# Kernel optimization log

Measured on AMD Instinct MI355X. Metric: run time of the kernel, lower is better.

Reference implementation:

```python
import jax, jax.numpy as jnp
import numpy as np

WS = 7      # window size
SHIFT = 3   # shift size
H = 56
W = 56
NH = 16     # num heads


def _layernorm(x, g, b):
    m = x.mean(-1, keepdims=True)
    v = x.var(-1, keepdims=True)
    return (x - m) / jnp.sqrt(v + 1e-5) * g + b


def setup_inputs() -> dict:
    key = jax.random.key(0)
    ks = jax.random.split(key, 8)
    B, C = 16, 512
    DH = 4 * C
    s = 0.02
    x = jax.random.normal(ks[0], (B, H * W, C), jnp.float32)

    # relative position index (matches torch buffer construction)
    coords = np.stack(np.meshgrid(np.arange(WS), np.arange(WS), indexing='ij')).reshape(2, -1)
    rel = (coords[:, :, None] - coords[:, None, :]).transpose(1, 2, 0).copy()
    rel[..., 0] += WS - 1
    rel[..., 1] += WS - 1
    rel[..., 0] *= 2 * WS - 1
    rpi = jnp.asarray(rel.sum(-1), jnp.int32)  # (49, 49)

    # shifted-window additive attention mask (nW, N, N)
    img = np.zeros((H, W))
    cnt = 0
    for hs in (slice(0, -WS), slice(-WS, -SHIFT), slice(-SHIFT, None)):
        for wsl in (slice(0, -WS), slice(-WS, -SHIFT), slice(-SHIFT, None)):
            img[hs, wsl] = cnt
            cnt += 1
    mw = img.reshape(H // WS, WS, W // WS, WS).transpose(0, 2, 1, 3).reshape(-1, WS * WS)
    diff = mw[:, None, :] - mw[:, :, None]  # == mw.unsqueeze(1) - mw.unsqueeze(2)
    attn_mask = jnp.asarray(np.where(diff != 0, -100.0, 0.0), jnp.float32)

    return {
        'x': x,
        'rpi': rpi,
        'attn_mask': attn_mask,
        'norm1_g': jnp.ones((C,), jnp.float32),
        'norm1_b': jnp.zeros((C,), jnp.float32),
        'qkv_w': jax.random.normal(ks[1], (3 * C, C), jnp.float32) * s,
        'qkv_b': jnp.zeros((3 * C,), jnp.float32),
        'proj_w': jax.random.normal(ks[2], (C, C), jnp.float32) * s,
        'proj_b': jnp.zeros((C,), jnp.float32),
        'rpb_table': jax.random.normal(ks[3], ((2 * WS - 1) ** 2, NH), jnp.float32) * s,
        'norm2_g': jnp.ones((C,), jnp.float32),
        'norm2_b': jnp.zeros((C,), jnp.float32),
        'mlp_w1': jax.random.normal(ks[4], (DH, C), jnp.float32) * s,
        'mlp_b1': jnp.zeros((DH,), jnp.float32),
        'mlp_w2': jax.random.normal(ks[5], (C, DH), jnp.float32) * s,
        'mlp_b2': jnp.zeros((C,), jnp.float32),
    }


def reference(x, rpi, attn_mask, norm1_g, norm1_b, qkv_w, qkv_b, proj_w, proj_b,
              rpb_table, norm2_g, norm2_b, mlp_w1, mlp_b1, mlp_w2, mlp_b2):
    B, L, C = x.shape
    N = WS * WS
    nW = (H // WS) * (W // WS)
    hd = C // NH

    # --- attention branch ---
    h = _layernorm(x, norm1_g, norm1_b).reshape(B, H, W, C)
    h = jnp.roll(h, (-SHIFT, -SHIFT), axis=(1, 2))
    # window partition -> (B*nW, N, C)
    xw = h.reshape(B, H // WS, WS, W // WS, WS, C).transpose(0, 1, 3, 2, 4, 5).reshape(B * nW, N, C)

    qkv = (xw @ qkv_w.T + qkv_b).reshape(B * nW, N, 3, NH, hd).transpose(2, 0, 3, 1, 4)
    q, k, v = qkv[0], qkv[1], qkv[2]  # (B*nW, NH, N, hd)
    attn = jnp.einsum('bhnd,bhmd->bhnm', q * (hd ** -0.5), k)
    rpb = rpb_table[rpi].transpose(2, 0, 1)  # (NH, N, N)
    attn = attn + rpb[None]
    attn = attn.reshape(B, nW, NH, N, N) + attn_mask[None, :, None]
    attn = jax.nn.softmax(attn.reshape(B * nW, NH, N, N), axis=-1)
    o = jnp.einsum('bhnm,bhmd->bhnd', attn, v).transpose(0, 2, 1, 3).reshape(B * nW, N, C)
    o = o @ proj_w.T + proj_b
    # window reverse + unshift
    o = o.reshape(B, H // WS, W // WS, WS, WS, C).transpose(0, 1, 3, 2, 4, 5).reshape(B, H, W, C)
    o = jnp.roll(o, (SHIFT, SHIFT), axis=(1, 2)).reshape(B, L, C)

    x = x + o
    # --- MLP branch ---
    h2 = _layernorm(x, norm2_g, norm2_b)
    m = jax.nn.gelu(h2 @ mlp_w1.T + mlp_b1, approximate=False)
    return x + (m @ mlp_w2.T + mlp_b2)
```

## Files before the change

kernel.cpp:

```cpp
#include <hip/hip_runtime.h>
#include <hip/hip_bf16.h>

typedef __attribute__((ext_vector_type(8))) short bf16x8_t;
typedef __attribute__((ext_vector_type(4))) float f32x4_t;

__device__ __forceinline__ void gll16(const void* g, void* l) {
  __builtin_amdgcn_global_load_lds((const __attribute__((address_space(1))) void*)g,
                                   (__attribute__((address_space(3))) void*)l, 16, 0, 0);
}

__global__ __launch_bounds__(256) void k_cvt4(const float* __restrict__ s0, const float* __restrict__ s1,
                                              const float* __restrict__ s2, const float* __restrict__ s3,
                                              __hip_bfloat16* __restrict__ out) {
  int i4 = blockIdx.x * 256 + threadIdx.x;
  int i = i4 * 4;
  const float* src;
  int off;
  if (i < 786432)       { src = s0; off = i; }
  else if (i < 1048576) { src = s1; off = i - 786432; }
  else if (i < 2097152) { src = s2; off = i - 1048576; }
  else                  { src = s3; off = i - 2097152; }
  float4 v = *(const float4*)(src + off);
  union { __hip_bfloat16 h[4]; ushort2 u2[2]; } pk;
  pk.h[0] = __float2bfloat16(v.x); pk.h[1] = __float2bfloat16(v.y);
  pk.h[2] = __float2bfloat16(v.z); pk.h[3] = __float2bfloat16(v.w);
  *(ushort2*)(out + i) = pk.u2[0];
  *(ushort2*)(out + i + 2) = pk.u2[1];
}

__global__ __launch_bounds__(256) void k_cmb(const int* __restrict__ rpi,
                                             const float* __restrict__ tab,
                                             const float* __restrict__ mask,
                                             float* __restrict__ cmbp) {
  int idx = blockIdx.x * 256 + threadIdx.x;
  int jj = idx & 3, lane = (idx >> 2) & 63, tile = (idx >> 8) & 15;
  int h = (idx >> 12) & 15, w6 = idx >> 16;
  int r = (tile >> 2) * 16 + (lane >> 4) * 4 + jj;
  int c = (tile & 3) * 16 + (lane & 15);
  float v = -1e9f;
  if (r < 49 && c < 49) v = tab[rpi[r * 49 + c] * 16 + h] + mask[w6 * 2401 + r * 49 + c];
  cmbp[idx] = v;
}

template<int PERM>
__global__ __launch_bounds__(256) void k_ln(const float* __restrict__ in,
                                            const float* __restrict__ g,
                                            const float* __restrict__ bta,
                                            __hip_bfloat16* __restrict__ out) {
  const int w = threadIdx.x >> 6, l = threadIdx.x & 63;
  const int token = blockIdx.x * 4 + w;
  const float4* p = (const float4*)(in + (size_t)token * 512);
  float4 v0 = p[l], v1 = p[l + 64];
  float s  = v0.x + v0.y + v0.z + v0.w + v1.x + v1.y + v1.z + v1.w;
  float sq = v0.x*v0.x + v0.y*v0.y + v0.z*v0.z + v0.w*v0.w
           + v1.x*v1.x + v1.y*v1.y + v1.z*v1.z + v1.w*v1.w;
  #pragma unroll
  for (int d = 1; d < 64; d <<= 1) { s += __shfl_xor(s, d); sq += __shfl_xor(sq, d); }
  float mean = s * (1.f / 512.f);
  float inv = rsqrtf(sq * (1.f / 512.f) - mean * mean + 1e-5f);
  size_t dst;
  if (PERM) {
    int b = token / 3136, pp = token - b * 3136;
    int i = pp / 56, j = pp - i * 56;
    int gi = (i + 53) % 56, gj = (j + 53) % 56;
    dst = ((size_t)(((b * 64) + (gi / 7) * 8 + (gj / 7)) * 49) + (gi % 7) * 7 + (gj % 7)) * 512;
  } else {
    dst = (size_t)token * 512;
  }
  int c0 = l * 4, c1 = 256 + l * 4;
  union { __hip_bfloat16 h[4]; ushort4 u4; } a, b4;
  a.h[0] = __float2bfloat16((v0.x - mean) * inv * g[c0]     + bta[c0]);
  a.h[1] = __float2bfloat16((v0.y - mean) * inv * g[c0 + 1] + bta[c0 + 1]);
  a.h[2] = __float2bfloat16((v0.z - mean) * inv * g[c0 + 2] + bta[c0 + 2]);
  a.h[3] = __float2bfloat16((v0.w - mean) * inv * g[c0 + 3] + bta[c0 + 3]);
  b4.h[0] = __float2bfloat16((v1.x - mean) * inv * g[c1]     + bta[c1]);
  b4.h[1] = __float2bfloat16((v1.y - mean) * inv * g[c1 + 1] + bta[c1 + 1]);
  b4.h[2] = __float2bfloat16((v1.z - mean) * inv * g[c1 + 2] + bta[c1 + 2]);
  b4.h[3] = __float2bfloat16((v1.w - mean) * inv * g[c1 + 3] + bta[c1 + 3]);
  *(ushort4*)(out + dst + c0) = a.u4;
  *(ushort4*)(out + dst + c1) = b4.u4;
}

__global__ __launch_bounds__(256) void k_attn(const __hip_bfloat16* __restrict__ qkv,
                                              const float* __restrict__ cmbp,
                                              __hip_bfloat16* __restrict__ o) {
  __shared__ __align__(16) __hip_bfloat16 vt_all[4 * 32 * 72];
  __shared__ __align__(16) __hip_bfloat16 P_all[4 * 64 * 72];
  const int t = threadIdx.x, l = t & 63, w = t >> 6;
  const int bw = blockIdx.x;
  const int head = blockIdx.y * 4 + w;
  const int rr = l & 15, g = l >> 4;
  __hip_bfloat16* vt = vt_all + w * (32 * 72);
  __hip_bfloat16* P  = P_all  + w * (64 * 72);
  const __hip_bfloat16* base = qkv + (size_t)bw * 49 * 1536 + head * 32;
  const bf16x8_t zero8 = {};

  { int d = l >> 1, sg = (l & 1) * 8;
    *(bf16x8_t*)(vt + d * 72 + 48 + sg) = zero8; }
  __builtin_amdgcn_sched_barrier(0);
  #pragma unroll
  for (int it = 0; it < 4; ++it) {
    int idx = l + it * 64;
    if (idx < 196) {
      int j = idx >> 2, sg = (idx & 3) * 8;
      bf16x8_t vv = *(const bf16x8_t*)(base + 1024 + (size_t)j * 1536 + sg);
      #pragma unroll
      for (int s2 = 0; s2 < 8; ++s2) vt[(sg + s2) * 72 + j] = ((__hip_bfloat16*)&vv)[s2];
    }
  }
  bf16x8_t aq[4], bk[4];
  #pragma unroll
  for (int m = 0; m < 4; ++m) {
    int row = m * 16 + rr;
    aq[m] = (row < 49) ? *(const bf16x8_t*)(base + (size_t)row * 1536 + g * 8) : zero8;
    bk[m] = (row < 49) ? *(const bf16x8_t*)(base + 512 + (size_t)row * 1536 + g * 8) : zero8;
  }
  const float4* cp = (const float4*)(cmbp + (size_t)((bw & 63) * 16 + head) * 4096);
  f32x4_t S[4][4];
  #pragma unroll
  for (int tm = 0; tm < 4; ++tm)
    #pragma unroll
    for (int tn = 0; tn < 4; ++tn) {
      float4 cv = cp[(tm * 4 + tn) * 64 + l];
      f32x4_t c0 = { cv.x, cv.y, cv.z, cv.w };
      S[tm][tn] = __builtin_amdgcn_mfma_f32_16x16x32_bf16(aq[tm], bk[tn], c0, 0, 0, 0);
    }
  float sm[4][4];
  #pragma unroll
  for (int tm = 0; tm < 4; ++tm) {
    #pragma unroll
    for (int jj = 0; jj < 4; ++jj) {
      float v = fmaxf(fmaxf(S[tm][0][jj], S[tm][1][jj]), fmaxf(S[tm][2][jj], S[tm][3][jj]));
      v = fmaxf(v, __shfl_xor(v, 1));
      v = fmaxf(v, __shfl_xor(v, 2));
      v = fmaxf(v, __shfl_xor(v, 4));
      v = fmaxf(v, __shfl_xor(v, 8));
      float s = 0.f;
      #pragma unroll
      for (int tn = 0; tn < 4; ++tn) {
        float e = __expf(S[tm][tn][jj] - v);
        S[tm][tn][jj] = e;
        s += e;
      }
      s += __shfl_xor(s, 1); s += __shfl_xor(s, 2); s += __shfl_xor(s, 4); s += __shfl_xor(s, 8);
      sm[tm][jj] = s;
    }
  }
  #pragma unroll
  for (int tm = 0; tm < 4; ++tm)
    #pragma unroll
    for (int tn = 0; tn < 4; ++tn)
      #pragma unroll
      for (int jj = 0; jj < 4; ++jj)
        P[(tm * 16 + g * 4 + jj) * 72 + tn * 16 + rr] = __float2bfloat16(S[tm][tn][jj]);

  f32x4_t O[4][2] = {};
  #pragma unroll
  for (int ks = 0; ks < 2; ++ks) {
    bf16x8_t pa[4], vb[2];
    #pragma unroll
    for (int tm = 0; tm < 4; ++tm)
      pa[tm] = *(const bf16x8_t*)(P + (tm * 16 + rr) * 72 + ks * 32 + g * 8);
    #pragma unroll
    for (int tn = 0; tn < 2; ++tn)
      vb[tn] = *(const bf16x8_t*)(vt + (tn * 16 + rr) * 72 + ks * 32 + g * 8);
    #pragma unroll
    for (int tm = 0; tm < 4; ++tm)
      #pragma unroll
      for (int tn = 0; tn < 2; ++tn)
        O[tm][tn] = __builtin_amdgcn_mfma_f32_16x16x32_bf16(pa[tm], vb[tn], O[tm][tn], 0, 0, 0);
  }
  #pragma unroll
  for (int tm = 0; tm < 4; ++tm) {
    #pragma unroll
    for (int jj = 0; jj < 4; ++jj) {
      int r = tm * 16 + g * 4 + jj;
      if (r < 49) {
        float rcp = 1.f / sm[tm][jj];
        size_t ob = ((size_t)bw * 49 + r) * 512 + head * 32;
        o[ob + rr]      = __float2bfloat16(O[tm][0][jj] * rcp);
        o[ob + 16 + rr] = __float2bfloat16(O[tm][1][jj] * rcp);
      }
    }
  }
}

template<int EP>
__global__ __launch_bounds__(512, 2) void gemm_w(const __hip_bfloat16* __restrict__ A,
                                                 const __hip_bfloat16* __restrict__ Bw,
                                                 int K, int Ncols, int nNB,
                                                 const float* __restrict__ bias,
                                                 __hip_bfloat16* __restrict__ obf,
                                                 const float* __restrict__ resid,
                                                 float* __restrict__ ofp) {
  __shared__ __align__(16) char LDS[163840];
  const int nwg = gridDim.x, orig = blockIdx.x;
  const int q8 = nwg >> 3, r8 = nwg & 7;
  const int xcd = orig & 7, lin = orig >> 3;
  const int wgid = (xcd < r8 ? xcd * (q8 + 1) : r8 * (q8 + 1) + (xcd - r8) * q8) + lin;
  const int bx = wgid / nNB, by = wgid - bx * nNB;
  const int m0 = bx * 128, n0 = by * 512;
  const int t = threadIdx.x, l = t & 63, w = t >> 6;
  const int rr = l & 15, kq = l >> 4;
  const int swzo = (kq * 16) ^ ((rr & 8) << 2);

  int rs0, cs0, rs1, cs1;
  { int d = t * 16;  rs0 = (d >> 10) * 16 + ((d >> 6) & 15);
    cs0 = ((d & 63) ^ (((d >> 9) & 1) << 5)) >> 1; }
  { int d = 8192 + t * 16; int dd = d & 8191;
    rs1 = (dd >> 10) * 16 + ((dd >> 6) & 15);
    cs1 = 32 + (((d & 63) ^ (((d >> 9) & 1) << 5)) >> 1); }
  const __hip_bfloat16* gA = A + (size_t)m0 * K;
  const __hip_bfloat16* gB = Bw + (size_t)n0 * K;

  auto stageA = [&](int T) {
    char* dst = LDS + (T & 1) * 16384 + t * 16;
    const size_t kb = (size_t)T * 64;
    gll16(gA + (size_t)rs0 * K + kb + cs0, dst);
    gll16(gA + (size_t)rs1 * K + kb + cs1, dst + 8192);
  };
  auto stageBu = [&](int T, int u) {
    char* dst = LDS + 32768 + (T & 1) * 65536 + u * 16384 + t * 16;
    const size_t kb = (size_t)T * 64;
    gll16(gB + (size_t)(u * 128 + rs0) * K + kb + cs0, dst);
    gll16(gB + (size_t)(u * 128 + rs1) * K + kb + cs1, dst + 8192);
  };

  auto ldA = [&](bf16x8_t (&a)[4][2], int buf, int mq) {
    const char* b = LDS + buf * 16384;
    #pragma unroll
    for (int m = 0; m < 4; ++m) {
      int r = mq * 64 + m * 16 + rr;
      #pragma unroll
      for (int ks = 0; ks < 2; ++ks)
        a[m][ks] = *(const bf16x8_t*)(b + ks * 8192 + (r >> 4) * 1024 + (r & 15) * 64 + swzo);
    }
  };
  auto ldB = [&](bf16x8_t (&bv)[2][2], int buf, int nq) {
    #pragma unroll
    for (int n = 0; n < 2; ++n) {
      int rB = w * 64 + (nq * 2 + n) * 16 + rr;
      const char* b = LDS + 32768 + buf * 65536 + (rB >> 7) * 16384;
      int r = rB & 127;
      #pragma unroll
      for (int ks = 0; ks < 2; ++ks)
        bv[n][ks] = *(const bf16x8_t*)(b + ks * 8192 + (r >> 4) * 1024 + (r & 15) * 64 + swzo);
    }
  };

  f32x4_t acc[8][4] = {};
  auto mma = [&](bf16x8_t (&a)[4][2], bf16x8_t (&bv)[2][2], int mq, int nq) {
    __builtin_amdgcn_s_setprio(1);
    #pragma unroll
    for (int m = 0; m < 4; ++m)
      #pragma unroll
      for (int n = 0; n < 2; ++n)
        #pragma unroll
        for (int ks = 0; ks < 2; ++ks)
          acc[mq * 4 + m][nq * 2 + n] =
            __builtin_amdgcn_mfma_f32_16x16x32_bf16(a[m][ks], bv[n][ks], acc[mq * 4 + m][nq * 2 + n], 0, 0, 0);
    __builtin_amdgcn_s_setprio(0);
  };

  const int NT = K >> 6;
  stageA(0); stageBu(0, 0); stageBu(0, 1); stageBu(0, 2); stageBu(0, 3);
  if (1 < NT) { stageBu(1, 0); stageBu(1, 1); }
  if (1 < NT) asm volatile("s_waitcnt vmcnt(4)" ::: "memory");
  else        asm volatile("s_waitcnt vmcnt(0)" ::: "memory");
  __builtin_amdgcn_s_barrier();

  for (int kt = 0; kt < NT; ++kt) {
    const int cur = kt & 1;
    const bool nx1 = (kt + 1 < NT), nx2 = (kt + 2 < NT);
    bf16x8_t Am0[4][2], Am1[4][2], Bn0[2][2], Bn1[2][2];
    ldA(Am0, cur, 0); ldB(Bn0, cur, 0);
    if (nx1) stageBu(kt + 1, 2);
    mma(Am0, Bn0, 0, 0);
    ldA(Am1, cur, 1); ldB(Bn1, cur, 1);
    if (nx1) stageBu(kt + 1, 3);
    mma(Am1, Bn0, 1, 0);
    __builtin_amdgcn_s_barrier();
    if (nx1) stageA(kt + 1);
    if (nx2) stageBu(kt + 2, 0);
    mma(Am1, Bn1, 1, 1);
    if (nx2) stageBu(kt + 2, 1);
    mma(Am0, Bn1, 0, 1);
    if (nx1) {
      if (nx2) asm volatile("s_waitcnt vmcnt(4)" ::: "memory");
      else     asm volatile("s_waitcnt vmcnt(0)" ::: "memory");
    }
    __builtin_amdgcn_s_barrier();
  }

  #pragma unroll
  for (int m = 0; m < 8; ++m) {
    #pragma unroll
    for (int j = 0; j < 4; ++j) {
      const int grow = m0 + m * 16 + kq * 4 + j;
      size_t rowbase;
      if (EP == 1) {
        int bw = grow / 49, nn = grow - bw * 49;
        int b = bw >> 6, wi = bw & 63;
        int hh = (wi >> 3) * 7 + nn / 7 + 3;  if (hh >= 56) hh -= 56;
        int ww2 = (wi & 7) * 7 + (nn % 7) + 3; if (ww2 >= 56) ww2 -= 56;
        rowbase = ((size_t)b * 3136 + hh * 56 + ww2) * 512;
      } else if (EP == 3) {
        rowbase = (size_t)grow * 512;
      } else {
        rowbase = (size_t)grow * Ncols;
      }
      #pragma unroll
      for (int n = 0; n < 4; ++n) {
        const int gcol = n0 + w * 64 + n * 16 + rr;
        float v = acc[m][n][j] + bias[gcol];
        if (EP == 0) {
          if (gcol < 512) v *= 0.17677669529663687f;
          obf[rowbase + gcol] = __float2bfloat16(v);
        } else if (EP == 1) {
          ofp[rowbase + gcol] = resid[rowbase + gcol] + v;
        } else if (EP == 2) {
          float u = 0.5f * v * (1.f + erff(v * 0.70710678118f));
          obf[rowbase + gcol] = __float2bfloat16(u);
        } else {
          ofp[rowbase + gcol] += v;
        }
      }
    }
  }
}

extern "C" void kernel_launch(void* const* d_in, const int* in_sizes, int n_in,
                              void* d_out, int out_size, void* d_ws, size_t ws_size,
                              hipStream_t stream) {
  const float* x      = (const float*)d_in[0];
  const int*   rpi    = (const int*)  d_in[1];
  const float* amask  = (const float*)d_in[2];
  const float* n1g    = (const float*)d_in[3];
  const float* n1b    = (const float*)d_in[4];
  const float* qkv_w  = (const float*)d_in[5];
  const float* qkv_b  = (const float*)d_in[6];
  const float* proj_w = (const float*)d_in[7];
  const float* proj_b = (const float*)d_in[8];
  const float* rpb_t  = (const float*)d_in[9];
  const float* n2g    = (const float*)d_in[10];
  const float* n2b    = (const float*)d_in[11];
  const float* w1     = (const float*)d_in[12];
  const float* b1     = (const float*)d_in[13];
  const float* w2     = (const float*)d_in[14];
  const float* b2     = (const float*)d_in[15];
  float* out = (float*)d_out;

  char* ws = (char*)d_ws;
  const size_t M = 50176;
  const size_t szA = M * 2048 * 2;
  const size_t szB = M * 1536 * 2;
  const size_t offB = szA;
  const size_t offW = offB + szB;
  __hip_bfloat16* bufA = (__hip_bfloat16*)(ws);
  __hip_bfloat16* bufB = (__hip_bfloat16*)(ws + offB);
  __hip_bfloat16* wqkv  = (__hip_bfloat16*)(ws + offW);
  float* cmbp = (float*)(ws + szA - (size_t)4194304 * 4);
  __hip_bfloat16* wproj = wqkv + 786432;
  __hip_bfloat16* wm1   = wproj + 262144;
  __hip_bfloat16* wm2   = wm1 + 1048576;

  k_cvt4<<<3072, 256, 0, stream>>>(qkv_w, proj_w, w1, w2, wqkv);
  k_cmb<<<16384, 256, 0, stream>>>(rpi, rpb_t, amask, cmbp);

  k_ln<1><<<12544, 256, 0, stream>>>(x, n1g, n1b, bufA);
  gemm_w<0><<<392 * 3, 512, 0, stream>>>(bufA, wqkv, 512, 1536, 3, qkv_b, bufB, nullptr, nullptr);
  k_attn<<<dim3(1024, 4), 256, 0, stream>>>(bufB, cmbp, bufA);
  gemm_w<1><<<392, 512, 0, stream>>>(bufA, wproj, 512, 512, 1, proj_b, nullptr, x, out);
  k_ln<0><<<12544, 256, 0, stream>>>(out, n2g, n2b, bufB);
  gemm_w<2><<<392 * 4, 512, 0, stream>>>(bufB, wm1, 512, 2048, 4, b1, bufA, nullptr, nullptr);
  gemm_w<3><<<392, 512, 0, stream>>>(bufA, wm2, 2048, 512, 1, b2, nullptr, nullptr, out);
}
```

Before: 777.6 us.

## Replace pipelined 128x512 GEMM with simple 128x128 single-buffered tile kernel

Swaps the double-buffered, software-pipelined 128x512 GEMM (512 threads, 160KB LDS) for a plain 128x128 tile kernel with 256 threads, 16KB LDS, a K step of 32 and a synchronous load, barrier, compute loop. The aim is more workgroups and higher occupancy from a smaller LDS footprint. The cost is less reuse per tile (more global traffic for B and A) and no overlap of loads with MFMA work. The XCD remap is also simplified and now assumes the grid size divides evenly by 8.

```diff
diff --git a/kernel.cpp b/kernel.cpp
--- a/kernel.cpp
+++ b/kernel.cpp
@@ -186,117 +186,61 @@
 }
 
 template<int EP>
-__global__ __launch_bounds__(512, 2) void gemm_w(const __hip_bfloat16* __restrict__ A,
-                                                 const __hip_bfloat16* __restrict__ Bw,
-                                                 int K, int Ncols, int nNB,
-                                                 const float* __restrict__ bias,
-                                                 __hip_bfloat16* __restrict__ obf,
-                                                 const float* __restrict__ resid,
-                                                 float* __restrict__ ofp) {
-  __shared__ __align__(16) char LDS[163840];
+__global__ __launch_bounds__(256) void gemm128(const __hip_bfloat16* __restrict__ A,
+                                               const __hip_bfloat16* __restrict__ Bw,
+                                               int K, int Ncols, int nNB,
+                                               const float* __restrict__ bias,
+                                               __hip_bfloat16* __restrict__ obf,
+                                               const float* __restrict__ resid,
+                                               float* __restrict__ ofp) {
+  __shared__ __align__(16) char Ash[8192];
+  __shared__ __align__(16) char Bsh[8192];
   const int nwg = gridDim.x, orig = blockIdx.x;
-  const int q8 = nwg >> 3, r8 = nwg & 7;
-  const int xcd = orig & 7, lin = orig >> 3;
-  const int wgid = (xcd < r8 ? xcd * (q8 + 1) : r8 * (q8 + 1) + (xcd - r8) * q8) + lin;
+  const int q8 = nwg >> 3;
+  const int wgid = (orig & 7) * q8 + (orig >> 3);
   const int bx = wgid / nNB, by = wgid - bx * nNB;
-  const int m0 = bx * 128, n0 = by * 512;
+  const int m0 = bx * 128, n0 = by * 128;
   const int t = threadIdx.x, l = t & 63, w = t >> 6;
+  const int wr = w >> 1, wc = w & 1;
   const int rr = l & 15, kq = l >> 4;
   const int swzo = (kq * 16) ^ ((rr & 8) << 2);
 
   int rs0, cs0, rs1, cs1;
-  { int d = t * 16;  rs0 = (d >> 10) * 16 + ((d >> 6) & 15);
+  { int d = t * 16;        rs0 = (d >> 10) * 16 + ((d >> 6) & 15);
     cs0 = ((d & 63) ^ (((d >> 9) & 1) << 5)) >> 1; }
-  { int d = 8192 + t * 16; int dd = d & 8191;
-    rs1 = (dd >> 10) * 16 + ((dd >> 6) & 15);
-    cs1 = 32 + (((d & 63) ^ (((d >> 9) & 1) << 5)) >> 1); }
+  { int d = 4096 + t * 16; rs1 = (d >> 10) * 16 + ((d >> 6) & 15);
+    cs1 = ((d & 63) ^ (((d >> 9) & 1) << 5)) >> 1; }
   const __hip_bfloat16* gA = A + (size_t)m0 * K;
   const __hip_bfloat16* gB = Bw + (size_t)n0 * K;
 
-  auto stageA = [&](int T) {
-    char* dst = LDS + (T & 1) * 16384 + t * 16;
-    const size_t kb = (size_t)T * 64;
-    gll16(gA + (size_t)rs0 * K + kb + cs0, dst);
-    gll16(gA + (size_t)rs1 * K + kb + cs1, dst + 8192);
-  };
-  auto stageBu = [&](int T, int u) {
-    char* dst = LDS + 32768 + (T & 1) * 65536 + u * 16384 + t * 16;
-    const size_t kb = (size_t)T * 64;
-    gll16(gB + (size_t)(u * 128 + rs0) * K + kb + cs0, dst);
-    gll16(gB + (size_t)(u * 128 + rs1) * K + kb + cs1, dst + 8192);
-  };
-
-  auto ldA = [&](bf16x8_t (&a)[4][2], int buf, int mq) {
-    const char* b = LDS + buf * 16384;
-    #pragma unroll
-    for (int m = 0; m < 4; ++m) {
-      int r = mq * 64 + m * 16 + rr;
-      #pragma unroll
-      for (int ks = 0; ks < 2; ++ks)
-        a[m][ks] = *(const bf16x8_t*)(b + ks * 8192 + (r >> 4) * 1024 + (r & 15) * 64 + swzo);
-    }
-  };
-  auto ldB = [&](bf16x8_t (&bv)[2][2], int buf, int nq) {
-    #pragma unroll
-    for (int n = 0; n < 2; ++n) {
-      int rB = w * 64 + (nq * 2 + n) * 16 + rr;
-      const char* b = LDS + 32768 + buf * 65536 + (rB >> 7) * 16384;
-      int r = rB & 127;
-      #pragma unroll
-      for (int ks = 0; ks < 2; ++ks)
-        bv[n][ks] = *(const bf16x8_t*)(b + ks * 8192 + (r >> 4) * 1024 + (r & 15) * 64 + swzo);
-    }
-  };
-
-  f32x4_t acc[8][4] = {};
-  auto mma = [&](bf16x8_t (&a)[4][2], bf16x8_t (&bv)[2][2], int mq, int nq) {
-    __builtin_amdgcn_s_setprio(1);
+  f32x4_t acc[4][4] = {};
+
+  for (int k0 = 0; k0 < K; k0 += 32) {
+    gll16(gA + (size_t)rs0 * K + k0 + cs0, Ash + t * 16);
+    gll16(gA + (size_t)rs1 * K + k0 + cs1, Ash + 4096 + t * 16);
+    gll16(gB + (size_t)rs0 * K + k0 + cs0, Bsh + t * 16);
+    gll16(gB + (size_t)rs1 * K + k0 + cs1, Bsh + 4096 + t * 16);
+    __syncthreads();
+    bf16x8_t af[4], bfr[4];
     #pragma unroll
     for (int m = 0; m < 4; ++m)
-      #pragma unroll
-      for (int n = 0; n < 2; ++n)
-        #pragma unroll
-        for (int ks = 0; ks < 2; ++ks)
-          acc[mq * 4 + m][nq * 2 + n] =
-            __builtin_amdgcn_mfma_f32_16x16x32_bf16(a[m][ks], bv[n][ks], acc[mq * 4 + m][nq * 2 + n], 0, 0, 0);
-    __builtin_amdgcn_s_setprio(0);
-  };
-
-  const int NT = K >> 6;
-  stageA(0); stageBu(0, 0); stageBu(0, 1); stageBu(0, 2); stageBu(0, 3);
-  if (1 < NT) { stageBu(1, 0); stageBu(1, 1); }
-  if (1 < NT) asm volatile("s_waitcnt vmcnt(4)" ::: "memory");
-  else        asm volatile("s_waitcnt vmcnt(0)" ::: "memory");
-  __builtin_amdgcn_s_barrier();
-
-  for (int kt = 0; kt < NT; ++kt) {
-    const int cur = kt & 1;
-    const bool nx1 = (kt + 1 < NT), nx2 = (kt + 2 < NT);
-    bf16x8_t Am0[4][2], Am1[4][2], Bn0[2][2], Bn1[2][2];
-    ldA(Am0, cur, 0); ldB(Bn0, cur, 0);
-    if (nx1) stageBu(kt + 1, 2);
-    mma(Am0, Bn0, 0, 0);
-    ldA(Am1, cur, 1); ldB(Bn1, cur, 1);
-    if (nx1) stageBu(kt + 1, 3);
-    mma(Am1, Bn0, 1, 0);
-    __builtin_amdgcn_s_barrier();
-    if (nx1) stageA(kt + 1);
-    if (nx2) stageBu(kt + 2, 0);
-    mma(Am1, Bn1, 1, 1);
-    if (nx2) stageBu(kt + 2, 1);
-    mma(Am0, Bn1, 0, 1);
-    if (nx1) {
-      if (nx2) asm volatile("s_waitcnt vmcnt(4)" ::: "memory");
-      else     asm volatile("s_waitcnt vmcnt(0)" ::: "memory");
-    }
-    __builtin_amdgcn_s_barrier();
-  }
-
-  #pragma unroll
-  for (int m = 0; m < 8; ++m) {
+      af[m] = *(const bf16x8_t*)(Ash + (wr * 4 + m) * 1024 + rr * 64 + swzo);
+    #pragma unroll
+    for (int n = 0; n < 4; ++n)
+      bfr[n] = *(const bf16x8_t*)(Bsh + (wc * 4 + n) * 1024 + rr * 64 + swzo);
+    #pragma unroll
+    for (int m = 0; m < 4; ++m)
+      #pragma unroll
+      for (int n = 0; n < 4; ++n)
+        acc[m][n] = __builtin_amdgcn_mfma_f32_16x16x32_bf16(af[m], bfr[n], acc[m][n], 0, 0, 0);
+    __syncthreads();
+  }
+
+  #pragma unroll
+  for (int m = 0; m < 4; ++m) {
     #pragma unroll
     for (int j = 0; j < 4; ++j) {
-      const int grow = m0 + m * 16 + kq * 4 + j;
+      const int grow = m0 + wr * 64 + m * 16 + kq * 4 + j;
       size_t rowbase;
       if (EP == 1) {
         int bw = grow / 49, nn = grow - bw * 49;
@@ -311,7 +255,7 @@
       }
       #pragma unroll
       for (int n = 0; n < 4; ++n) {
-        const int gcol = n0 + w * 64 + n * 16 + rr;
+        const int gcol = n0 + wc * 64 + n * 16 + rr;
         float v = acc[m][n][j] + bias[gcol];
         if (EP == 0) {
           if (gcol < 512) v *= 0.17677669529663687f;
@@ -368,10 +312,10 @@
   k_cmb<<<16384, 256, 0, stream>>>(rpi, rpb_t, amask, cmbp);
 
   k_ln<1><<<12544, 256, 0, stream>>>(x, n1g, n1b, bufA);
-  gemm_w<0><<<392 * 3, 512, 0, stream>>>(bufA, wqkv, 512, 1536, 3, qkv_b, bufB, nullptr, nullptr);
+  gemm128<0><<<392 * 12, 256, 0, stream>>>(bufA, wqkv, 512, 1536, 12, qkv_b, bufB, nullptr, nullptr);
   k_attn<<<dim3(1024, 4), 256, 0, stream>>>(bufB, cmbp, bufA);
-  gemm_w<1><<<392, 512, 0, stream>>>(bufA, wproj, 512, 512, 1, proj_b, nullptr, x, out);
+  gemm128<1><<<392 * 4, 256, 0, stream>>>(bufA, wproj, 512, 512, 4, proj_b, nullptr, x, out);
   k_ln<0><<<12544, 256, 0, stream>>>(out, n2g, n2b, bufB);
-  gemm_w<2><<<392 * 4, 512, 0, stream>>>(bufB, wm1, 512, 2048, 4, b1, bufA, nullptr, nullptr);
-  gemm_w<3><<<392, 512, 0, stream>>>(bufA, wm2, 2048, 512, 1, b2, nullptr, nullptr, out);
-}
+  gemm128<2><<<392 * 16, 256, 0, stream>>>(bufB, wm1, 512, 2048, 16, b1, bufA, nullptr, nullptr);
+  gemm128<3><<<392 * 4, 256, 0, stream>>>(bufA, wm2, 2048, 512, 4, b2, nullptr, nullptr, out);
+}
```

After: 775.3 us. No clear change (-0.3%).
